# Kernel tuning notes

Hardware: AMD Instinct MI355X
Metric: run time of the kernel (lower is better)

Reference implementation:

```python
import jax, jax.numpy as jnp
import numpy as np

G, K1, K2, N, NP, EPS = 16, 128, 32, 128, 512, 1e-5

def _bn(x, axes):
    m = jnp.mean(x, axes, keepdims=True)
    v = jnp.var(x, axes, keepdims=True)  # biased, as torch BN training mode
    return (x - m) * jax.lax.rsqrt(v + EPS)

def _fps(xyz, npoint):
    # farthest point sampling, deterministic start at index 0; xyz (B,P,3)
    B, P, _ = xyz.shape
    def step(carry, _):
        dists, far = carry
        c = jnp.take_along_axis(xyz, far[:, None, None], axis=1)   # (B,1,3)
        d = jnp.sum((xyz - c) ** 2, -1)                            # (B,P)
        dists = jnp.minimum(dists, d)
        return (dists, jnp.argmax(dists, -1)), far
    init = (jnp.full((B, P), 1e10, xyz.dtype), jnp.zeros((B,), jnp.int32))
    _, idx = jax.lax.scan(step, init, None, length=npoint)         # (npoint,B)
    return jnp.take_along_axis(xyz, idx.T[:, :, None], axis=1)     # (B,npoint,3)

def _pointnet(x, w1, b1, w2, b2, w3, b3):
    h = jax.nn.relu(_bn(x @ w1 + b1, (0, 1)))
    h = jax.nn.relu(_bn(h @ w2 + b2, (0, 1)))
    h = _bn(h @ w3 + b3, (0, 1))
    return jnp.max(h, axis=1)                                      # (B,1024)

def _mapping(feat, w1, b1, w2, b2, w3, b3, w4, b4):
    # all 16 branches stacked on leading axis g
    h = jax.nn.relu(_bn(jnp.einsum('bk,gkj->gbj', feat, w1) + b1[:, None, :], (1,)))
    h = jax.nn.relu(_bn(jnp.einsum('gbj,gjk->gbk', h, w2) + b2[:, None, :], (1,)))
    h = jax.nn.relu(_bn(jnp.einsum('gbj,gjk->gbk', h, w3) + b3[:, None, :], (1,)))
    return jax.nn.relu(_bn(jnp.einsum('gbj,gjk->gbk', h, w4) + b4[:, None, :], (1,)))

def _axform(feat, fw, fb, c1w, c1b, c2w, c2b, c3w, c3b, c4w, c4b):
    # feat (G,B,K1); 1x1 convs expressed as einsums in channels-last layout
    xb = (jnp.einsum('gbk,gkm->gbm', feat, fw) + fb[:, None, :]).reshape(G, -1, N, K2)
    h = jax.nn.relu(_bn(jnp.einsum('gbnk,gkc->gbnc', xb, c1w) + c1b[:, None, None, :], (1, 2)))
    h = jax.nn.relu(_bn(jnp.einsum('gbnc,gcd->gbnd', h, c2w) + c2b[:, None, None, :], (1, 2)))
    h = jnp.einsum('gbnd,gde->gbne', h, c3w) + c3b[:, None, None, :]  # (G,B,N,1024)
    w = jax.nn.softmax(h, axis=2)                                     # softmax over N
    y = jnp.einsum('gbne,gbnk->gbek', w, xb)                          # (G,B,1024,K2)
    return jnp.einsum('gbek,gkc->gbec', y, c4w) + c4b[:, None, None, :]  # (G,B,1024,3)

def _forward(x, pn, mp, gen, ref):
    x_partial = _fps(x, NP)                                           # (B,512,3)
    feat = _pointnet(x, *pn)                                          # (B,1024)
    mfeat = _mapping(feat, *mp)                                       # (G,B,K1)
    x1g = _axform(mfeat, *gen)                                        # (G,B,1024,3)
    B = x.shape[0]
    x_1 = jnp.transpose(x1g, (1, 0, 2, 3)).reshape(B, -1, 3)          # (B,16384,3)
    fps1 = jax.vmap(lambda p: _fps(p, NP))(x1g)                       # (G,B,512,3)
    x_base = jnp.concatenate([fps1, jnp.broadcast_to(x_partial, (G,) + x_partial.shape)], axis=2)
    x2g = x_base + _axform(mfeat, *ref)                               # (G,B,1024,3)
    x_2 = jnp.transpose(x2g, (1, 0, 2, 3)).reshape(B, -1, 3)
    return x_1, x_2

def setup_inputs() -> dict:
    keys = iter(jax.random.split(jax.random.key(0), 40))
    def rn(shape, s=0.02):
        return (s * jax.random.normal(next(keys), shape)).astype(jnp.float32)
    inp = {}
    inp['x'] = jax.random.normal(next(keys), (16, 2048, 3), jnp.float32)
    inp['pn_w1'] = rn((3, 64));      inp['pn_b1'] = rn((64,))
    inp['pn_w2'] = rn((64, 128));    inp['pn_b2'] = rn((128,))
    inp['pn_w3'] = rn((128, 1024));  inp['pn_b3'] = rn((1024,))
    inp['mp_w1'] = rn((G, 1024, 1024)); inp['mp_b1'] = rn((G, 1024))
    inp['mp_w2'] = rn((G, 1024, 1024)); inp['mp_b2'] = rn((G, 1024))
    inp['mp_w3'] = rn((G, 1024, 1024)); inp['mp_b3'] = rn((G, 1024))
    inp['mp_w4'] = rn((G, 1024, K1));   inp['mp_b4'] = rn((G, K1))
    for p in ('g', 'r'):
        inp[p + '_fw'] = rn((G, K1, N * K2)); inp[p + '_fb'] = rn((G, N * K2))
        inp[p + '_c1w'] = rn((G, K2, 64));    inp[p + '_c1b'] = rn((G, 64))
        inp[p + '_c2w'] = rn((G, 64, 128));   inp[p + '_c2b'] = rn((G, 128))
        inp[p + '_c3w'] = rn((G, 128, 1024)); inp[p + '_c3b'] = rn((G, 1024))
        inp[p + '_c4w'] = rn((G, K2, 3));     inp[p + '_c4b'] = rn((G, 3))
    return inp

def reference(x, pn_w1, pn_b1, pn_w2, pn_b2, pn_w3, pn_b3,
              mp_w1, mp_b1, mp_w2, mp_b2, mp_w3, mp_b3, mp_w4, mp_b4,
              g_fw, g_fb, g_c1w, g_c1b, g_c2w, g_c2b, g_c3w, g_c3b, g_c4w, g_c4b,
              r_fw, r_fb, r_c1w, r_c1b, r_c2w, r_c2b, r_c3w, r_c3b, r_c4w, r_c4b):
    pn = (pn_w1, pn_b1, pn_w2, pn_b2, pn_w3, pn_b3)
    mp = (mp_w1, mp_b1, mp_w2, mp_b2, mp_w3, mp_b3, mp_w4, mp_b4)
    gen = (g_fw, g_fb, g_c1w, g_c1b, g_c2w, g_c2b, g_c3w, g_c3b, g_c4w, g_c4b)
    ref = (r_fw, r_fb, r_c1w, r_c1b, r_c2w, r_c2b, r_c3w, r_c3b, r_c4w, r_c4b)
    return _forward(x, pn, mp, gen, ref)
```

## Files before the change

kernel.cpp:

```cpp
#include <hip/hip_runtime.h>
#include <math.h>

#define TID ((int)threadIdx.x)

namespace {
constexpr float EPSf = 1e-5f;

typedef __attribute__((ext_vector_type(8))) short short8;
typedef __attribute__((ext_vector_type(4))) float f32x4;

struct FpsArgs {
  const float* pts; float* out; float* dmin; int* far;
  int it0, it1, nc;
};

__device__ __forceinline__ unsigned fenc(float f){
  unsigned u = __float_as_uint(f);
  return (u & 0x80000000u) ? ~u : (u | 0x80000000u);
}
__device__ __forceinline__ float fdec(unsigned e){
  unsigned u = (e & 0x80000000u) ? (e & 0x7fffffffu) : ~e;
  return __uint_as_float(u);
}
__device__ __forceinline__ short bf16rne(float f){
  unsigned u = __float_as_uint(f);
  return (short)((u + 0x7fffu + ((u >> 16) & 1u)) >> 16);
}

template<int CTRL>
__device__ __forceinline__ void dpp_comb(float& bm, int& bp){
  int om_i = __builtin_amdgcn_update_dpp(__float_as_int(bm), __float_as_int(bm), CTRL, 0xf, 0xf, false);
  int op   = __builtin_amdgcn_update_dpp(bp, bp, CTRL, 0xf, 0xf, false);
  float om = __int_as_float(om_i);
  if (om > bm || (om == bm && op < bp)){ bm = om; bp = op; }
}

template<int LP, int NT>
__device__ void fps_body(const FpsArgs& a, int ci){
  const int NPTS = NT*LP;
  const float* pts = a.pts + (size_t)ci * NPTS * 3;
  float* out = a.out + (size_t)ci * 512 * 3;
  float* dst = a.dmin + (size_t)ci * NPTS;
  float px[LP], py[LP], pz[LP], dmin[LP];
#pragma unroll
  for (int j = 0; j < LP; j++){
    int p = TID + NT*j;
    px[j] = pts[p*3+0]; py[j] = pts[p*3+1]; pz[j] = pts[p*3+2];
  }
  int far;
  if (a.it0 == 0){
#pragma unroll
    for (int j = 0; j < LP; j++) dmin[j] = 1e10f;
    far = 0;
  } else {
#pragma unroll
    for (int j = 0; j < LP; j++) dmin[j] = dst[TID + NT*j];
    far = a.far[ci];
  }
  __shared__ unsigned long long red2[2][NT/64];
  for (int i = a.it0; i < a.it1; i++){
    float cx = pts[far*3+0], cy = pts[far*3+1], cz = pts[far*3+2];
    if (TID == 0){ out[i*3+0]=cx; out[i*3+1]=cy; out[i*3+2]=cz; }
    float bm = -1.f; int bp = 0;
#pragma unroll
    for (int j = 0; j < LP; j++){
      float dx = __fsub_rn(px[j], cx);
      float dy = __fsub_rn(py[j], cy);
      float dz = __fsub_rn(pz[j], cz);
      float d  = __fadd_rn(__fadd_rn(__fmul_rn(dx,dx), __fmul_rn(dy,dy)), __fmul_rn(dz,dz));
      float dm = fminf(dmin[j], d);
      dmin[j] = dm;
      if (dm > bm){ bm = dm; bp = TID + NT*j; }
    }
    dpp_comb<0x111>(bm,bp); dpp_comb<0x112>(bm,bp); dpp_comb<0x114>(bm,bp);
    dpp_comb<0x118>(bm,bp); dpp_comb<0x142>(bm,bp); dpp_comb<0x143>(bm,bp);
    unsigned long long key =
      ((unsigned long long)(unsigned)__builtin_amdgcn_readlane(__float_as_int(bm), 63) << 32)
      | (unsigned)~(unsigned)__builtin_amdgcn_readlane(bp, 63);
    if ((TID & 63) == 63) red2[i&1][TID>>6] = key;
    __syncthreads();
    unsigned long long kk = red2[i&1][0];
#pragma unroll
    for (int t = 1; t < NT/64; t++){
      unsigned long long o = red2[i&1][t];
      kk = kk > o ? kk : o;
    }
    far = (int)~(unsigned)kk;
  }
  if (a.it1 < 512){
#pragma unroll
    for (int j = 0; j < LP; j++) dst[TID + NT*j] = dmin[j];
    if (TID == 0) a.far[ci] = far;
  }
}

template<int C, int K, int FLP>
__global__ void __launch_bounds__(256) rowgemm_kernel(const float* __restrict__ in,
    const float* __restrict__ w, const float* __restrict__ bias, const float2* __restrict__ st2,
    float* __restrict__ out, int rows_per_g, FpsArgs fa)
{
  int bid = blockIdx.x;
  if constexpr (FLP > 0){
    if (bid < fa.nc){ fps_body<FLP,256>(fa, bid); return; }
    bid -= fa.nc;
  }
  constexpr int RPB = 256 / C;
  __shared__ float lin[RPB * K];
  size_t row0 = (size_t)bid * RPB;
  int g = (int)(row0 / rows_per_g);
  for (int i = TID; i < RPB*K; i += 256){
    float v = in[row0*(size_t)K + i];
    if (st2){ float2 s = st2[(size_t)g*K + (i % K)]; v = fmaxf((v - s.x)*s.y, 0.f); }
    lin[i] = v;
  }
  __syncthreads();
  int r = TID / C, c = TID % C;
  float acc = bias[(size_t)g*C + c];
  const float* wg = w + (size_t)g*K*C + c;
#pragma unroll
  for (int k = 0; k < K; k++) acc = fmaf(lin[r*K + k], wg[(size_t)k*C], acc);
  out[(row0 + r)*C + c] = acc;
}

template<int FLP>
__global__ void __launch_bounds__(256, 4) big1024b_kernel(const float* __restrict__ in,
    const float* __restrict__ w, const float* __restrict__ bias, const float2* __restrict__ st2,
    float* __restrict__ ps, float* __restrict__ pq, unsigned* __restrict__ maxenc, FpsArgs fa)
{
  int bid = blockIdx.x;
  if constexpr (FLP > 0){
    if (bid < fa.nc){ fps_body<FLP,256>(fa, bid); return; }
    bid -= fa.nc;
  }
  int rb = bid >> 1, ch = bid & 1;
  size_t row0 = (size_t)rb * 32;
  __shared__ float linT[4096];
  for (int i = TID; i < 4096; i += 256){
    int r = i >> 7, k = i & 127;
    float v = in[(row0 + r)*128 + k];
    float2 s = st2[k];
    linT[k*32 + r] = fmaxf((v - s.x)*s.y, 0.f);
  }
  __syncthreads();
  int rq = TID >> 6, cq = TID & 63;
  int c0 = ch*512 + cq*8;
  float acc[8][8];
  {
    float4 b0 = *(const float4*)(bias + c0);
    float4 b1 = *(const float4*)(bias + c0 + 4);
    const float bv[8] = {b0.x,b0.y,b0.z,b0.w,b1.x,b1.y,b1.z,b1.w};
#pragma unroll
    for (int ri = 0; ri < 8; ri++)
#pragma unroll
      for (int ci = 0; ci < 8; ci++) acc[ri][ci] = bv[ci];
  }
  const float* wp = w + c0;
#pragma unroll 2
  for (int k = 0; k < 128; k++){
    float4 w0 = *(const float4*)(wp + (size_t)k*1024);
    float4 w1 = *(const float4*)(wp + (size_t)k*1024 + 4);
    float4 l0 = *(const float4*)&linT[k*32 + rq*8];
    float4 l1 = *(const float4*)&linT[k*32 + rq*8 + 4];
    const float lv[8] = {l0.x,l0.y,l0.z,l0.w,l1.x,l1.y,l1.z,l1.w};
    const float wv[8] = {w0.x,w0.y,w0.z,w0.w,w1.x,w1.y,w1.z,w1.w};
#pragma unroll
    for (int ri = 0; ri < 8; ri++)
#pragma unroll
      for (int ci = 0; ci < 8; ci++)
        acc[ri][ci] = fmaf(lv[ri], wv[ci], acc[ri][ci]);
  }
  float s[8], q[8], m[8];
#pragma unroll
  for (int ci = 0; ci < 8; ci++){
    s[ci] = 0.f; q[ci] = 0.f; m[ci] = -1e38f;
#pragma unroll
    for (int ri = 0; ri < 8; ri++){
      float v = acc[ri][ci];
      s[ci] += v; q[ci] = fmaf(v, v, q[ci]); m[ci] = fmaxf(m[ci], v);
    }
  }
  __syncthreads();
  float* red = linT;
#pragma unroll
  for (int ci = 0; ci < 8; ci++){
    red[rq*512 + cq*8 + ci]        = s[ci];
    red[2048 + rq*512 + cq*8 + ci] = q[ci];
  }
  __syncthreads();
  if (rq == 0){
#pragma unroll
    for (int ci = 0; ci < 8; ci++){
      float ss = 0.f, qq = 0.f;
#pragma unroll
      for (int r = 0; r < 4; r++){
        ss += red[r*512 + cq*8 + ci];
        qq += red[2048 + r*512 + cq*8 + ci];
      }
      ps[(size_t)rb*1024 + c0 + ci] = ss;
      pq[(size_t)rb*1024 + c0 + ci] = qq;
    }
  }
  __syncthreads();
#pragma unroll
  for (int ci = 0; ci < 8; ci++) red[rq*512 + cq*8 + ci] = m[ci];
  __syncthreads();
  if (rq == 0){
    int b = (int)(row0 / 2048);
#pragma unroll
    for (int ci = 0; ci < 8; ci++){
      float mm = red[cq*8 + ci];
#pragma unroll
      for (int r = 1; r < 4; r++) mm = fmaxf(mm, red[r*512 + cq*8 + ci]);
      atomicMax(&maxenc[(size_t)b*1024 + c0 + ci], fenc(mm));
    }
  }
}

template<int FLP>
__global__ void __launch_bounds__(128) mapgemm2_kernel(const float* __restrict__ in, int in_gstride,
    const float* __restrict__ w, const float* __restrict__ bias, const float2* __restrict__ st2,
    float* __restrict__ out, int K, int J, int JB, int NS, FpsArgs fa)
{
  int bid = blockIdx.x;
  if constexpr (FLP > 0){
    if (bid < fa.nc){ fps_body<FLP,128>(fa, bid); return; }
    bid -= fa.nc;
  }
  int kc = bid / (JB*16);
  int g  = (bid / JB) % 16;
  int jb = bid % JB;
  int kchunk = K / NS, k0 = kc*kchunk;
  __shared__ float linT[128*16];
  const float* ing = in + (size_t)g * in_gstride;
  for (int i = TID; i < kchunk*16; i += 128){
    int b = i / kchunk, k = i - b*kchunk;
    float v = ing[(size_t)b*K + k0 + k];
    if (st2){ float2 s = st2[(size_t)g*K + k0 + k]; v = fmaxf((v - s.x)*s.y, 0.f); }
    linT[k*16 + b] = v;
  }
  __syncthreads();
  int bh = TID >> 6, jq = TID & 63;
  int j = jb*256 + jq*4;
  const float* wp = w + ((size_t)g*K + k0)*J + j;
  float4 a4[8];
#pragma unroll
  for (int bi = 0; bi < 8; bi++) a4[bi] = make_float4(0.f,0.f,0.f,0.f);
#pragma unroll 4
  for (int k = 0; k < kchunk; k++){
    float4 wv = *(const float4*)(wp + (size_t)k*J);
    float4 l0 = *(const float4*)&linT[k*16 + bh*8];
    float4 l1 = *(const float4*)&linT[k*16 + bh*8 + 4];
    const float lv[8] = {l0.x,l0.y,l0.z,l0.w,l1.x,l1.y,l1.z,l1.w};
#pragma unroll
    for (int bi = 0; bi < 8; bi++){
      a4[bi].x = fmaf(lv[bi], wv.x, a4[bi].x);
      a4[bi].y = fmaf(lv[bi], wv.y, a4[bi].y);
      a4[bi].z = fmaf(lv[bi], wv.z, a4[bi].z);
      a4[bi].w = fmaf(lv[bi], wv.w, a4[bi].w);
    }
  }
  if (NS == 1){
    float4 bv = *(const float4*)(bias + (size_t)g*J + j);
#pragma unroll
    for (int bi = 0; bi < 8; bi++){
      int b = bh*8 + bi;
      float4 o = make_float4(a4[bi].x+bv.x, a4[bi].y+bv.y, a4[bi].z+bv.z, a4[bi].w+bv.w);
      *(float4*)&out[((size_t)g*16 + b)*J + j] = o;
    }
  } else {
#pragma unroll
    for (int bi = 0; bi < 8; bi++)
      *(float4*)&out[(((size_t)kc*16 + g)*16 + bh*8 + bi)*J + j] = a4[bi];
  }
}

__global__ void __launch_bounds__(256) mapgemm_kernel(const float* __restrict__ in, int in_gstride,
    const float* __restrict__ w, const float* __restrict__ bias, const float2* __restrict__ st2,
    float* __restrict__ out, int K, int J, int JB, int NS)
{
  int bid = blockIdx.x;
  int kc = bid / (JB*16);
  int g  = (bid / JB) % 16;
  int jb = bid % JB;
  int j  = jb*256 + TID;
  bool jv = j < J;
  int jc = jv ? j : 0;
  int kchunk = K / NS;
  int k0 = kc * kchunk;
  __shared__ float lin[16 * 128];
  const float* ing = in + (size_t)g * in_gstride;
  float acc[16];
  float bv = (NS == 1 && jv) ? bias[(size_t)g*J + jc] : 0.f;
#pragma unroll
  for (int b = 0; b < 16; b++) acc[b] = bv;
  for (int kt = k0; kt < k0 + kchunk; kt += 128){
    __syncthreads();
    for (int i = TID; i < 2048; i += 256){
      int b = i >> 7, k = i & 127;
      float v = ing[(size_t)b*K + kt + k];
      if (st2){ float2 s = st2[(size_t)g*K + kt + k]; v = fmaxf((v - s.x)*s.y, 0.f); }
      lin[i] = v;
    }
    __syncthreads();
    const float* wg = w + ((size_t)g*K + kt)*J + jc;
    for (int k = 0; k < 128; k++){
      float wv = wg[(size_t)k*J];
#pragma unroll
      for (int b = 0; b < 16; b++) acc[b] = fmaf(lin[b*128 + k], wv, acc[b]);
    }
  }
  if (jv){
    if (NS == 1){
      for (int b = 0; b < 16; b++) out[((size_t)g*16 + b)*J + j] = acc[b];
    } else {
      for (int b = 0; b < 16; b++) out[(((size_t)kc*16 + g)*16 + b)*J + j] = acc[b];
    }
  }
}

__global__ void __launch_bounds__(256) redstats_kernel(const float* __restrict__ part,
    const float* __restrict__ bias, float* __restrict__ out, float2* __restrict__ st2,
    int J, int NS)
{
  int t = blockIdx.x*256 + TID;
  int g = t / J, j = t % J;
  float bv = bias[t];
  float s = 0.f, q = 0.f;
  for (int b = 0; b < 16; b++){
    float v = bv;
    for (int c = 0; c < NS; c++) v += part[(((size_t)c*16 + g)*16 + b)*J + j];
    out[((size_t)g*16 + b)*J + j] = v;
    s += v; q = fmaf(v, v, q);
  }
  float mean = s * (1.f/16.f);
  float var  = q * (1.f/16.f) - mean*mean;
  st2[t] = make_float2(mean, rsqrtf(fmaxf(var, 0.f) + EPSf));
}

template<int FLP>
__global__ void __launch_bounds__(256) statsacc_kernel(const float* __restrict__ in,
    float* __restrict__ part, int C, size_t chunk, FpsArgs fa)
{
  int bid = blockIdx.x;
  if constexpr (FLP > 0){
    if (bid < fa.nc){ fps_body<FLP,256>(fa, bid); return; }
    bid -= fa.nc;
  }
  size_t base = (size_t)bid * chunk;
  int c = TID % C;
  float s = 0.f, q = 0.f;
  for (size_t idx = base + TID; idx < base + chunk; idx += 256){
    float v = in[idx]; s += v; q = fmaf(v, v, q);
  }
  __shared__ float ls[256], lq[256];
  ls[TID] = s; lq[TID] = q; __syncthreads();
  if (TID < C){
    for (int t = TID + C; t < 256; t += C){ s += ls[t]; q += lq[t]; }
    part[((size_t)bid*C + c)*2]   = s;
    part[((size_t)bid*C + c)*2+1] = q;
  }
}

__global__ void statsfin_kernel(const float* __restrict__ part, float2* __restrict__ st2,
    int C, int G, float invR)
{
  int slot = blockIdx.x*256 + TID;
  if (slot >= G*C) return;
  int g = slot / C, c = slot % C;
  int bpg = 256 / G;
  float s = 0.f, q = 0.f;
  for (int b = 0; b < bpg; b++){
    size_t p = ((size_t)(g*bpg + b)*C + c)*2;
    s += part[p]; q += part[p+1];
  }
  float mean = s*invR;
  float var  = q*invR - mean*mean;
  st2[slot] = make_float2(mean, rsqrtf(fmaxf(var, 0.f) + EPSf));
}

__global__ void pnfin_kernel(const float* __restrict__ ps, const float* __restrict__ pq,
                             float2* __restrict__ st)
{
  int c = blockIdx.x*256 + TID;
  float s = 0.f, q = 0.f;
  for (int rb = 0; rb < 1024; rb++){ s += ps[rb*1024 + c]; q += pq[rb*1024 + c]; }
  float mean = s * (1.f/32768.f);
  float var  = q * (1.f/32768.f) - mean*mean;
  st[c] = make_float2(mean, rsqrtf(fmaxf(var, 0.f) + EPSf));
}

__global__ void feat_kernel(const unsigned* __restrict__ me, const float2* __restrict__ st,
                            float* __restrict__ feat)
{
  int t = blockIdx.x*256 + TID;
  int c = t & 1023;
  float2 s = st[c];
  feat[t] = (fdec(me[t]) - s.x) * s.y;
}

__global__ void __launch_bounds__(256) wtr_kernel(const float* __restrict__ c3w,
                                                  short* __restrict__ wt)
{
  int g = blockIdx.x >> 4, kt = blockIdx.x & 15;
  __shared__ float lds[8*1024];
  const float* src = c3w + ((size_t)g*128 + kt*8)*1024;
  for (int i = TID; i < 8192; i += 256) lds[i] = src[i];
  __syncthreads();
  for (int e = TID; e < 1024; e += 256){
    short8 v;
#pragma unroll
    for (int j = 0; j < 8; j++) v[j] = bf16rne(lds[j*1024 + e]);
    *(short8*)&wt[((size_t)g*1024 + e)*128 + kt*8] = v;
  }
}

template<int FLP>
__global__ void __launch_bounds__(256, 3) fused_kernel(const float* __restrict__ c2o,
    const float2* __restrict__ st2, const short* __restrict__ wt,
    const float* __restrict__ xb, const float* __restrict__ c4w, const float* __restrict__ c4b,
    float* __restrict__ out_pts, float* __restrict__ out_x1, FpsArgs fa)
{
  int bid = blockIdx.x;
  if constexpr (FLP > 0){
    if (bid < fa.nc){ fps_body<FLP,256>(fa, bid); return; }
    bid -= fa.nc;
  }
  int gb = bid >> 3, eb = bid & 7;
  int g = gb >> 4, b = gb & 15;
  __shared__ short Abf[16384];
  __shared__ short xbT[4096];
  __shared__ float mred[512];
  __shared__ float sred[128];

  {
    const float* xsrc = xb + (size_t)gb*4096;
    for (int idx = TID; idx < 1024; idx += 256){
      int n = idx >> 3, k4 = (idx & 7)*4;
      float4 v = *(const float4*)(xsrc + n*32 + k4);
      const float vv[4] = {v.x, v.y, v.z, v.w};
#pragma unroll
      for (int j = 0; j < 4; j++){
        int k = k4 + j;
        xbT[k*128 + (((n >> 3) ^ (k & 7)) << 3) + (n & 7)] = bf16rne(vv[j]);
      }
    }
  }
  const float* src = c2o + (size_t)gb*16384;
  for (int i = TID; i < 2048; i += 256){
    int n = i >> 4, kc = i & 15;
    float4 a0 = *(const float4*)(src + n*128 + kc*8);
    float4 a1 = *(const float4*)(src + n*128 + kc*8 + 4);
    const float vals[8] = {a0.x,a0.y,a0.z,a0.w,a1.x,a1.y,a1.z,a1.w};
    short8 ob;
#pragma unroll
    for (int j = 0; j < 8; j++){
      float2 s = st2[(size_t)g*128 + kc*8 + j];
      ob[j] = bf16rne(fmaxf((vals[j] - s.x)*s.y, 0.f));
    }
    *(short8*)&Abf[n*128 + ((kc ^ (n & 7)) << 3)] = ob;
  }
  __syncthreads();

  int lane = TID & 63, wid = TID >> 6;
  int lr = lane & 15, lkg = lane >> 4;

  f32x4 acc[2][8];
#pragma unroll
  for (int nt = 0; nt < 2; nt++)
#pragma unroll
    for (int et = 0; et < 8; et++) acc[nt][et] = (f32x4){0.f,0.f,0.f,0.f};
  const short* wtg = wt + ((size_t)g*1024 + eb*128)*128;
#pragma unroll
  for (int kt = 0; kt < 4; kt++){
    int kb = kt*32 + lkg*8;
    int kcf = kb >> 3;
    short8 afr[2];
#pragma unroll
    for (int nt = 0; nt < 2; nt++){
      int row = wid*32 + nt*16 + lr;
      afr[nt] = *(const short8*)&Abf[row*128 + ((kcf ^ (row & 7)) << 3)];
    }
#pragma unroll
    for (int et = 0; et < 8; et++){
      short8 bfr = *(const short8*)&wtg[(et*16 + lr)*128 + kb];
      acc[0][et] = __builtin_amdgcn_mfma_f32_16x16x32_bf16(afr[0], bfr, acc[0][et], 0, 0, 0);
      acc[1][et] = __builtin_amdgcn_mfma_f32_16x16x32_bf16(afr[1], bfr, acc[1][et], 0, 0, 0);
    }
  }

  float m[8];
#pragma unroll
  for (int et = 0; et < 8; et++){
    float mm = -1e38f;
#pragma unroll
    for (int nt = 0; nt < 2; nt++)
#pragma unroll
      for (int r = 0; r < 4; r++) mm = fmaxf(mm, acc[nt][et][r]);
    mm = fmaxf(mm, __shfl_xor(mm, 16));
    mm = fmaxf(mm, __shfl_xor(mm, 32));
    m[et] = mm;
  }
  if (lkg == 0){
#pragma unroll
    for (int et = 0; et < 8; et++) mred[wid*128 + et*16 + lr] = m[et];
  }
  __syncthreads();
#pragma unroll
  for (int et = 0; et < 8; et++){
    float mm = fmaxf(fmaxf(mred[et*16 + lr],       mred[128 + et*16 + lr]),
                     fmaxf(mred[256 + et*16 + lr], mred[384 + et*16 + lr]));
    m[et] = mm;
  }

  float sp[8];
  unsigned* Pu = (unsigned*)Abf;
#pragma unroll
  for (int et = 0; et < 8; et++){
    float ss = 0.f;
#pragma unroll
    for (int nt = 0; nt < 2; nt++)
#pragma unroll
      for (int r = 0; r < 4; r++){
        float p = __expf(acc[nt][et][r] - m[et]);
        acc[nt][et][r] = p;
        ss += p;
      }
    ss += __shfl_xor(ss, 16);
    ss += __shfl_xor(ss, 32);
    sp[et] = ss;
    int e = et*16 + lr;
#pragma unroll
    for (int nt = 0; nt < 2; nt++){
      int nb = wid*32 + nt*16 + lkg*4;
      int base = e*128 + ((((nb >> 3)) ^ (e & 7)) << 3) + (nb & 7);
      unsigned lo = (unsigned)(unsigned short)bf16rne(acc[nt][et][0])
                  | ((unsigned)(unsigned short)bf16rne(acc[nt][et][1]) << 16);
      unsigned hi = (unsigned)(unsigned short)bf16rne(acc[nt][et][2])
                  | ((unsigned)(unsigned short)bf16rne(acc[nt][et][3]) << 16);
      Pu[base >> 1]       = lo;
      Pu[(base >> 1) + 1] = hi;
    }
  }
  __syncthreads();
  if (lkg == 0){
#pragma unroll
    for (int et = 0; et < 8; et++) mred[wid*128 + et*16 + lr] = sp[et];
  }
  __syncthreads();
  if (wid == 0){
#pragma unroll
    for (int t = 0; t < 2; t++){
      int e = t*64 + lane;
      float s = mred[e] + mred[128 + e] + mred[256 + e] + mred[384 + e];
      sred[e] = 1.f / s;
    }
  }

  f32x4 yy[2][2];
#pragma unroll
  for (int t2 = 0; t2 < 2; t2++){ yy[t2][0] = (f32x4){0.f,0.f,0.f,0.f}; yy[t2][1] = (f32x4){0.f,0.f,0.f,0.f}; }
#pragma unroll
  for (int nc = 0; nc < 4; nc++){
    short8 bfrs[2];
#pragma unroll
    for (int kt2 = 0; kt2 < 2; kt2++){
      int k = kt2*16 + lr;
      bfrs[kt2] = *(const short8*)&xbT[k*128 + (((nc*4 + lkg) ^ (k & 7)) << 3)];
    }
#pragma unroll
    for (int t2 = 0; t2 < 2; t2++){
      int e = (wid*2 + t2)*16 + lr;
      short8 afr = *(const short8*)&Abf[e*128 + (((nc*4 + lkg) ^ (e & 7)) << 3)];
      yy[t2][0] = __builtin_amdgcn_mfma_f32_16x16x32_bf16(afr, bfrs[0], yy[t2][0], 0, 0, 0);
      yy[t2][1] = __builtin_amdgcn_mfma_f32_16x16x32_bf16(afr, bfrs[1], yy[t2][1], 0, 0, 0);
    }
  }
  __syncthreads();

  float c4l[2][3];
  {
    const float* cw = c4w + g*96;
#pragma unroll
    for (int kt2 = 0; kt2 < 2; kt2++){
      int k = kt2*16 + lr;
      c4l[kt2][0] = cw[k*3+0]; c4l[kt2][1] = cw[k*3+1]; c4l[kt2][2] = cw[k*3+2];
    }
  }
  float cb0 = c4b[g*3+0], cb1 = c4b[g*3+1], cb2 = c4b[g*3+2];
#pragma unroll
  for (int t2 = 0; t2 < 2; t2++){
#pragma unroll
    for (int r = 0; r < 4; r++){
      float o0 = yy[t2][0][r]*c4l[0][0] + yy[t2][1][r]*c4l[1][0];
      float o1 = yy[t2][0][r]*c4l[0][1] + yy[t2][1][r]*c4l[1][1];
      float o2 = yy[t2][0][r]*c4l[0][2] + yy[t2][1][r]*c4l[1][2];
#pragma unroll
      for (int d = 1; d < 16; d <<= 1){
        o0 += __shfl_xor(o0, d);
        o1 += __shfl_xor(o1, d);
        o2 += __shfl_xor(o2, d);
      }
      if (lr == 0){
        int e = (wid*2 + t2)*16 + lkg*4 + r;
        float rs = sred[e];
        o0 = fmaf(o0, rs, cb0);
        o1 = fmaf(o1, rs, cb1);
        o2 = fmaf(o2, rs, cb2);
        int eg = eb*128 + e;
        size_t po = ((size_t)gb*1024 + eg)*3;
        out_pts[po+0] = o0; out_pts[po+1] = o1; out_pts[po+2] = o2;
        if (out_x1){
          size_t xo = (((size_t)b*16 + g)*1024 + eg)*3;
          out_x1[xo+0] = o0; out_x1[xo+1] = o1; out_x1[xo+2] = o2;
        }
      }
    }
  }
}

__global__ void combine_kernel(const float* __restrict__ fps1, const float* __restrict__ xpart,
                               const float* __restrict__ d2, float* __restrict__ x2)
{
  size_t i = (size_t)blockIdx.x*256 + TID;
  if (i >= (size_t)16*16*1024*3) return;
  int c = (int)(i % 3);
  size_t t = i / 3;
  int e = (int)(t % 1024);
  size_t gb = t / 1024;
  int g = (int)(gb >> 4), b = (int)(gb & 15);
  float base;
  if (e < 512) base = fps1[(gb*512 + e)*3 + c];
  else         base = xpart[((size_t)b*512 + (e - 512))*3 + c];
  x2[(((size_t)b*16384) + (size_t)g*1024 + e)*3 + c] = base + d2[i];
}

}

extern "C" void kernel_launch(void* const* d_in, const int* in_sizes, int n_in,
                              void* d_out, int out_size, void* d_ws, size_t ws_size,
                              hipStream_t stream)
{
  (void)in_sizes; (void)n_in; (void)out_size; (void)ws_size;
  const float* x    = (const float*)d_in[0];
  const float* pnw1 = (const float*)d_in[1];
  const float* pnb1 = (const float*)d_in[2];
  const float* pnw2 = (const float*)d_in[3];
  const float* pnb2 = (const float*)d_in[4];
  const float* pnw3 = (const float*)d_in[5];
  const float* pnb3 = (const float*)d_in[6];
  const float* mpw[4] = {(const float*)d_in[7],(const float*)d_in[9],(const float*)d_in[11],(const float*)d_in[13]};
  const float* mpb[4] = {(const float*)d_in[8],(const float*)d_in[10],(const float*)d_in[12],(const float*)d_in[14]};

  float* ws = (float*)d_ws;
  size_t o = 0;
  auto alloc = [&](size_t n){ float* p = ws + o; o += n; return p; };
  float* x_partial = alloc(24576);
  float* feat      = alloc(16384);
  float* mfeat     = alloc(32768);
  float2* st_pn1   = (float2*)alloc(128);
  float2* st_pn2   = (float2*)alloc(256);
  float2* st_pn3   = (float2*)alloc(2048);
  float2* st_c1    = (float2*)alloc(2048);
  float2* st_c2    = (float2*)alloc(4096);
  float2* st_map0  = (float2*)alloc(32768);
  float2* st_map1  = (float2*)alloc(32768);
  float2* st_map2  = (float2*)alloc(32768);
  float2* st_map3  = (float2*)alloc(4096);
  float* sa_part   = alloc(65536);
  float* pn_ps     = alloc(1048576);
  float* pn_pq     = alloc(1048576);
  unsigned* maxenc = (unsigned*)alloc(16384);
  float* mapA      = alloc(262144);
  float* mapB      = alloc(262144);
  float* mpart     = alloc(4194304);
  float* xb        = alloc(1048576);
  float* c1o       = alloc(2097152);
  float* c2o       = alloc(4194304);
  float* x1g       = alloc(786432);
  float* d2buf     = alloc(786432);
  float* fps1b     = alloc(393216);
  float* fpsA_dmin = alloc(32768);
  int*   fpsA_far  = (int*)alloc(16);
  float* fpsB_dmin = alloc(262144);
  int*   fpsB_far  = (int*)alloc(256);
  short* wt_g      = (short*)alloc(1048576);
  short* wt_r      = (short*)alloc(1048576);

  float* xout1 = (float*)d_out;
  float* xout2 = xout1 + 786432;

  hipMemsetAsync(maxenc, 0, 16384*sizeof(unsigned), stream);

  wtr_kernel<<<256, 256, 0, stream>>>((const float*)d_in[21], wt_g);
  wtr_kernel<<<256, 256, 0, stream>>>((const float*)d_in[31], wt_r);

  FpsArgs f0{};
  FpsArgs fa{x, x_partial, fpsA_dmin, fpsA_far, 0, 0, 16};

  fa.it0 = 0; fa.it1 = 64;
  rowgemm_kernel<64,3,8><<<8192+16, 256, 0, stream>>>(x, pnw1, pnb1, nullptr, c1o, 32768, fa);
  statsacc_kernel<0><<<256, 256, 0, stream>>>(c1o, sa_part, 64, 8192, f0);
  statsfin_kernel<<<1, 256, 0, stream>>>(sa_part, st_pn1, 64, 1, 1.f/32768.f);
  fa.it0 = 64; fa.it1 = 128;
  rowgemm_kernel<128,64,8><<<16384+16, 256, 0, stream>>>(c1o, pnw2, pnb2, st_pn1, c2o, 32768, fa);
  statsacc_kernel<0><<<256, 256, 0, stream>>>(c2o, sa_part, 128, 16384, f0);
  statsfin_kernel<<<1, 256, 0, stream>>>(sa_part, st_pn2, 128, 1, 1.f/32768.f);
  fa.it0 = 128; fa.it1 = 224;
  big1024b_kernel<8><<<2048+16, 256, 0, stream>>>(c2o, pnw3, pnb3, st_pn2,
                                                  pn_ps, pn_pq, maxenc, fa);
  pnfin_kernel<<<4, 256, 0, stream>>>(pn_ps, pn_pq, st_pn3);
  feat_kernel<<<64, 256, 0, stream>>>(maxenc, st_pn3, feat);

  fa.it0 = 224; fa.it1 = 288;
  mapgemm2_kernel<16><<<1024+16, 128, 0, stream>>>(feat, 0,     mpw[0], nullptr, nullptr, mpart, 1024, 1024, 4, 16, fa);
  redstats_kernel<<<64, 256, 0, stream>>>(mpart, mpb[0], mapA, st_map0, 1024, 16);
  fa.it0 = 288; fa.it1 = 352;
  mapgemm2_kernel<16><<<1024+16, 128, 0, stream>>>(mapA, 16384, mpw[1], nullptr, st_map0, mpart, 1024, 1024, 4, 16, fa);
  redstats_kernel<<<64, 256, 0, stream>>>(mpart, mpb[1], mapB, st_map1, 1024, 16);
  fa.it0 = 352; fa.it1 = 416;
  mapgemm2_kernel<16><<<1024+16, 128, 0, stream>>>(mapB, 16384, mpw[2], nullptr, st_map1, mpart, 1024, 1024, 4, 16, fa);
  redstats_kernel<<<64, 256, 0, stream>>>(mpart, mpb[2], mapA, st_map2, 1024, 16);
  mapgemm_kernel<<<64, 256, 0, stream>>>(mapA, 16384, mpw[3], nullptr, st_map2, mpart, 1024, 128, 1, 4);
  redstats_kernel<<<8, 256, 0, stream>>>(mpart, mpb[3], mfeat, st_map3, 128, 4);

  for (int p = 0; p < 2; p++){
    const float* fw  = (const float*)d_in[15 + p*10 + 0];
    const float* fb  = (const float*)d_in[15 + p*10 + 1];
    const float* c1w = (const float*)d_in[15 + p*10 + 2];
    const float* c1b = (const float*)d_in[15 + p*10 + 3];
    const float* c2w = (const float*)d_in[15 + p*10 + 4];
    const float* c2b = (const float*)d_in[15 + p*10 + 5];
    const float* c4w = (const float*)d_in[15 + p*10 + 8];
    const float* c4b = (const float*)d_in[15 + p*10 + 9];

    if (p == 0){
      fa.it0 = 416; fa.it1 = 480;
      mapgemm2_kernel<16><<<256+16, 128, 0, stream>>>(mfeat, 2048, fw, fb, st_map3, xb, 128, 4096, 16, 1, fa);
      fa.it0 = 480; fa.it1 = 512;
      rowgemm_kernel<64,32,8><<<8192+16, 256, 0, stream>>>(xb, c1w, c1b, nullptr, c1o, 2048, fa);
      statsacc_kernel<0><<<256, 256, 0, stream>>>(c1o, sa_part, 64, 8192, f0);
      statsfin_kernel<<<4, 256, 0, stream>>>(sa_part, st_c1, 64, 16, 1.f/2048.f);
      rowgemm_kernel<128,64,0><<<16384, 256, 0, stream>>>(c1o, c2w, c2b, st_c1, c2o, 2048, f0);
      statsacc_kernel<0><<<256, 256, 0, stream>>>(c2o, sa_part, 128, 16384, f0);
      statsfin_kernel<<<8, 256, 0, stream>>>(sa_part, st_c2, 128, 16, 1.f/2048.f);
      fused_kernel<0><<<2048, 256, 0, stream>>>(c2o, st_c2, wt_g, xb, c4w, c4b, x1g, xout1, f0);
    } else {
      FpsArgs fb_{x1g, fps1b, fpsB_dmin, fpsB_far, 0, 0, 256};
      mapgemm2_kernel<0><<<256, 128, 0, stream>>>(mfeat, 2048, fw, fb, st_map3, xb, 128, 4096, 16, 1, f0);
      fb_.it0 = 0; fb_.it1 = 72;
      rowgemm_kernel<64,32,4><<<8192+256, 256, 0, stream>>>(xb, c1w, c1b, nullptr, c1o, 2048, fb_);
      fb_.it0 = 72; fb_.it1 = 104;
      statsacc_kernel<4><<<256+256, 256, 0, stream>>>(c1o, sa_part, 64, 8192, fb_);
      statsfin_kernel<<<4, 256, 0, stream>>>(sa_part, st_c1, 64, 16, 1.f/2048.f);
      fb_.it0 = 104; fb_.it1 = 208;
      rowgemm_kernel<128,64,4><<<16384+256, 256, 0, stream>>>(c1o, c2w, c2b, st_c1, c2o, 2048, fb_);
      fb_.it0 = 208; fb_.it1 = 240;
      statsacc_kernel<4><<<256+256, 256, 0, stream>>>(c2o, sa_part, 128, 16384, fb_);
      statsfin_kernel<<<8, 256, 0, stream>>>(sa_part, st_c2, 128, 16, 1.f/2048.f);
      fb_.it0 = 240; fb_.it1 = 512;
      fused_kernel<4><<<2048+256, 256, 0, stream>>>(c2o, st_c2, wt_r, xb, c4w, c4b, d2buf, nullptr, fb_);
    }
  }

  combine_kernel<<<3072, 256, 0, stream>>>(fps1b, x_partial, d2buf, xout2);
}
```

Baseline: 1.794 ms.

## Loop fused kernel over all e-blocks per gb and rebalance FPS overlap

```diff
diff --git a/kernel.cpp b/kernel.cpp
--- a/kernel.cpp
+++ b/kernel.cpp
@@ -425,13 +425,15 @@
     if (bid < fa.nc){ fps_body<FLP,256>(fa, bid); return; }
     bid -= fa.nc;
   }
-  int gb = bid >> 3, eb = bid & 7;
+  int gb = bid;
   int g = gb >> 4, b = gb & 15;
-  __shared__ short Abf[16384];
+  __shared__ short Pbf[16384];
   __shared__ short xbT[4096];
+  __shared__ float2 sb[128];
   __shared__ float mred[512];
   __shared__ float sred[128];
 
+  if (TID < 128) sb[TID] = st2[(size_t)g*128 + TID];
   {
     const float* xsrc = xb + (size_t)gb*4096;
     for (int idx = TID; idx < 1024; idx += 256){
@@ -445,137 +447,32 @@
       }
     }
   }
-  const float* src = c2o + (size_t)gb*16384;
-  for (int i = TID; i < 2048; i += 256){
-    int n = i >> 4, kc = i & 15;
-    float4 a0 = *(const float4*)(src + n*128 + kc*8);
-    float4 a1 = *(const float4*)(src + n*128 + kc*8 + 4);
-    const float vals[8] = {a0.x,a0.y,a0.z,a0.w,a1.x,a1.y,a1.z,a1.w};
-    short8 ob;
-#pragma unroll
-    for (int j = 0; j < 8; j++){
-      float2 s = st2[(size_t)g*128 + kc*8 + j];
-      ob[j] = bf16rne(fmaxf((vals[j] - s.x)*s.y, 0.f));
-    }
-    *(short8*)&Abf[n*128 + ((kc ^ (n & 7)) << 3)] = ob;
-  }
   __syncthreads();
 
   int lane = TID & 63, wid = TID >> 6;
   int lr = lane & 15, lkg = lane >> 4;
 
-  f32x4 acc[2][8];
-#pragma unroll
-  for (int nt = 0; nt < 2; nt++)
-#pragma unroll
-    for (int et = 0; et < 8; et++) acc[nt][et] = (f32x4){0.f,0.f,0.f,0.f};
-  const short* wtg = wt + ((size_t)g*1024 + eb*128)*128;
+  short8 afr[4][2];
+  const float* src = c2o + (size_t)gb*16384;
 #pragma unroll
   for (int kt = 0; kt < 4; kt++){
     int kb = kt*32 + lkg*8;
-    int kcf = kb >> 3;
-    short8 afr[2];
+    float2 ss[8];
+#pragma unroll
+    for (int j = 0; j < 8; j++) ss[j] = sb[kb + j];
 #pragma unroll
     for (int nt = 0; nt < 2; nt++){
       int row = wid*32 + nt*16 + lr;
-      afr[nt] = *(const short8*)&Abf[row*128 + ((kcf ^ (row & 7)) << 3)];
-    }
-#pragma unroll
-    for (int et = 0; et < 8; et++){
-      short8 bfr = *(const short8*)&wtg[(et*16 + lr)*128 + kb];
-      acc[0][et] = __builtin_amdgcn_mfma_f32_16x16x32_bf16(afr[0], bfr, acc[0][et], 0, 0, 0);
-      acc[1][et] = __builtin_amdgcn_mfma_f32_16x16x32_bf16(afr[1], bfr, acc[1][et], 0, 0, 0);
-    }
-  }
-
-  float m[8];
-#pragma unroll
-  for (int et = 0; et < 8; et++){
-    float mm = -1e38f;
-#pragma unroll
-    for (int nt = 0; nt < 2; nt++)
-#pragma unroll
-      for (int r = 0; r < 4; r++) mm = fmaxf(mm, acc[nt][et][r]);
-    mm = fmaxf(mm, __shfl_xor(mm, 16));
-    mm = fmaxf(mm, __shfl_xor(mm, 32));
-    m[et] = mm;
-  }
-  if (lkg == 0){
-#pragma unroll
-    for (int et = 0; et < 8; et++) mred[wid*128 + et*16 + lr] = m[et];
-  }
-  __syncthreads();
-#pragma unroll
-  for (int et = 0; et < 8; et++){
-    float mm = fmaxf(fmaxf(mred[et*16 + lr],       mred[128 + et*16 + lr]),
-                     fmaxf(mred[256 + et*16 + lr], mred[384 + et*16 + lr]));
-    m[et] = mm;
-  }
-
-  float sp[8];
-  unsigned* Pu = (unsigned*)Abf;
-#pragma unroll
-  for (int et = 0; et < 8; et++){
-    float ss = 0.f;
-#pragma unroll
-    for (int nt = 0; nt < 2; nt++)
-#pragma unroll
-      for (int r = 0; r < 4; r++){
-        float p = __expf(acc[nt][et][r] - m[et]);
-        acc[nt][et][r] = p;
-        ss += p;
-      }
-    ss += __shfl_xor(ss, 16);
-    ss += __shfl_xor(ss, 32);
-    sp[et] = ss;
-    int e = et*16 + lr;
-#pragma unroll
-    for (int nt = 0; nt < 2; nt++){
-      int nb = wid*32 + nt*16 + lkg*4;
-      int base = e*128 + ((((nb >> 3)) ^ (e & 7)) << 3) + (nb & 7);
-      unsigned lo = (unsigned)(unsigned short)bf16rne(acc[nt][et][0])
-                  | ((unsigned)(unsigned short)bf16rne(acc[nt][et][1]) << 16);
-      unsigned hi = (unsigned)(unsigned short)bf16rne(acc[nt][et][2])
-                  | ((unsigned)(unsigned short)bf16rne(acc[nt][et][3]) << 16);
-      Pu[base >> 1]       = lo;
-      Pu[(base >> 1) + 1] = hi;
-    }
-  }
-  __syncthreads();
-  if (lkg == 0){
-#pragma unroll
-    for (int et = 0; et < 8; et++) mred[wid*128 + et*16 + lr] = sp[et];
-  }
-  __syncthreads();
-  if (wid == 0){
-#pragma unroll
-    for (int t = 0; t < 2; t++){
-      int e = t*64 + lane;
-      float s = mred[e] + mred[128 + e] + mred[256 + e] + mred[384 + e];
-      sred[e] = 1.f / s;
-    }
-  }
-
-  f32x4 yy[2][2];
-#pragma unroll
-  for (int t2 = 0; t2 < 2; t2++){ yy[t2][0] = (f32x4){0.f,0.f,0.f,0.f}; yy[t2][1] = (f32x4){0.f,0.f,0.f,0.f}; }
-#pragma unroll
-  for (int nc = 0; nc < 4; nc++){
-    short8 bfrs[2];
-#pragma unroll
-    for (int kt2 = 0; kt2 < 2; kt2++){
-      int k = kt2*16 + lr;
-      bfrs[kt2] = *(const short8*)&xbT[k*128 + (((nc*4 + lkg) ^ (k & 7)) << 3)];
-    }
-#pragma unroll
-    for (int t2 = 0; t2 < 2; t2++){
-      int e = (wid*2 + t2)*16 + lr;
-      short8 afr = *(const short8*)&Abf[e*128 + (((nc*4 + lkg) ^ (e & 7)) << 3)];
-      yy[t2][0] = __builtin_amdgcn_mfma_f32_16x16x32_bf16(afr, bfrs[0], yy[t2][0], 0, 0, 0);
-      yy[t2][1] = __builtin_amdgcn_mfma_f32_16x16x32_bf16(afr, bfrs[1], yy[t2][1], 0, 0, 0);
-    }
-  }
-  __syncthreads();
+      float4 a0 = *(const float4*)(src + row*128 + kb);
+      float4 a1 = *(const float4*)(src + row*128 + kb + 4);
+      const float vals[8] = {a0.x,a0.y,a0.z,a0.w,a1.x,a1.y,a1.z,a1.w};
+      short8 ob;
+#pragma unroll
+      for (int j = 0; j < 8; j++)
+        ob[j] = bf16rne(fmaxf((vals[j] - ss[j].x)*ss[j].y, 0.f));
+      afr[kt][nt] = ob;
+    }
+  }
 
   float c4l[2][3];
   {
@@ -587,31 +484,139 @@
     }
   }
   float cb0 = c4b[g*3+0], cb1 = c4b[g*3+1], cb2 = c4b[g*3+2];
-#pragma unroll
-  for (int t2 = 0; t2 < 2; t2++){
-#pragma unroll
-    for (int r = 0; r < 4; r++){
-      float o0 = yy[t2][0][r]*c4l[0][0] + yy[t2][1][r]*c4l[1][0];
-      float o1 = yy[t2][0][r]*c4l[0][1] + yy[t2][1][r]*c4l[1][1];
-      float o2 = yy[t2][0][r]*c4l[0][2] + yy[t2][1][r]*c4l[1][2];
-#pragma unroll
-      for (int d = 1; d < 16; d <<= 1){
-        o0 += __shfl_xor(o0, d);
-        o1 += __shfl_xor(o1, d);
-        o2 += __shfl_xor(o2, d);
+  unsigned* Pu = (unsigned*)Pbf;
+
+  for (int eb = 0; eb < 8; eb++){
+    f32x4 acc[2][8];
+#pragma unroll
+    for (int nt = 0; nt < 2; nt++)
+#pragma unroll
+      for (int et = 0; et < 8; et++) acc[nt][et] = (f32x4){0.f,0.f,0.f,0.f};
+    const short* wtg = wt + ((size_t)g*1024 + eb*128)*128;
+#pragma unroll
+    for (int kt = 0; kt < 4; kt++){
+      int kb = kt*32 + lkg*8;
+#pragma unroll
+      for (int et = 0; et < 8; et++){
+        short8 bfr = *(const short8*)&wtg[(et*16 + lr)*128 + kb];
+        acc[0][et] = __builtin_amdgcn_mfma_f32_16x16x32_bf16(afr[kt][0], bfr, acc[0][et], 0, 0, 0);
+        acc[1][et] = __builtin_amdgcn_mfma_f32_16x16x32_bf16(afr[kt][1], bfr, acc[1][et], 0, 0, 0);
       }
-      if (lr == 0){
-        int e = (wid*2 + t2)*16 + lkg*4 + r;
-        float rs = sred[e];
-        o0 = fmaf(o0, rs, cb0);
-        o1 = fmaf(o1, rs, cb1);
-        o2 = fmaf(o2, rs, cb2);
-        int eg = eb*128 + e;
-        size_t po = ((size_t)gb*1024 + eg)*3;
-        out_pts[po+0] = o0; out_pts[po+1] = o1; out_pts[po+2] = o2;
-        if (out_x1){
-          size_t xo = (((size_t)b*16 + g)*1024 + eg)*3;
-          out_x1[xo+0] = o0; out_x1[xo+1] = o1; out_x1[xo+2] = o2;
+    }
+
+    float m[8];
+#pragma unroll
+    for (int et = 0; et < 8; et++){
+      float mm = -1e38f;
+#pragma unroll
+      for (int nt = 0; nt < 2; nt++)
+#pragma unroll
+        for (int r = 0; r < 4; r++) mm = fmaxf(mm, acc[nt][et][r]);
+      mm = fmaxf(mm, __shfl_xor(mm, 16));
+      mm = fmaxf(mm, __shfl_xor(mm, 32));
+      m[et] = mm;
+    }
+    if (lkg == 0){
+#pragma unroll
+      for (int et = 0; et < 8; et++) mred[wid*128 + et*16 + lr] = m[et];
+    }
+    __syncthreads();
+#pragma unroll
+    for (int et = 0; et < 8; et++){
+      m[et] = fmaxf(fmaxf(mred[et*16 + lr],       mred[128 + et*16 + lr]),
+                    fmaxf(mred[256 + et*16 + lr], mred[384 + et*16 + lr]));
+    }
+
+    float sp[8];
+#pragma unroll
+    for (int et = 0; et < 8; et++){
+      float ss = 0.f;
+#pragma unroll
+      for (int nt = 0; nt < 2; nt++)
+#pragma unroll
+        for (int r = 0; r < 4; r++){
+          float p = __expf(acc[nt][et][r] - m[et]);
+          acc[nt][et][r] = p;
+          ss += p;
+        }
+      ss += __shfl_xor(ss, 16);
+      ss += __shfl_xor(ss, 32);
+      sp[et] = ss;
+      int e = et*16 + lr;
+#pragma unroll
+      for (int nt = 0; nt < 2; nt++){
+        int nb = wid*32 + nt*16 + lkg*4;
+        int base = e*128 + ((((nb >> 3)) ^ (e & 7)) << 3) + (nb & 7);
+        unsigned lo = (unsigned)(unsigned short)bf16rne(acc[nt][et][0])
+                    | ((unsigned)(unsigned short)bf16rne(acc[nt][et][1]) << 16);
+        unsigned hi = (unsigned)(unsigned short)bf16rne(acc[nt][et][2])
+                    | ((unsigned)(unsigned short)bf16rne(acc[nt][et][3]) << 16);
+        Pu[base >> 1]       = lo;
+        Pu[(base >> 1) + 1] = hi;
+      }
+    }
+    __syncthreads();
+    if (lkg == 0){
+#pragma unroll
+      for (int et = 0; et < 8; et++) mred[wid*128 + et*16 + lr] = sp[et];
+    }
+    __syncthreads();
+    if (wid == 0){
+#pragma unroll
+      for (int t = 0; t < 2; t++){
+        int e = t*64 + lane;
+        float s = mred[e] + mred[128 + e] + mred[256 + e] + mred[384 + e];
+        sred[e] = 1.f / s;
+      }
+    }
+
+    f32x4 yy[2][2];
+#pragma unroll
+    for (int t2 = 0; t2 < 2; t2++){ yy[t2][0] = (f32x4){0.f,0.f,0.f,0.f}; yy[t2][1] = (f32x4){0.f,0.f,0.f,0.f}; }
+#pragma unroll
+    for (int nc = 0; nc < 4; nc++){
+      short8 bfrs[2];
+#pragma unroll
+      for (int kt2 = 0; kt2 < 2; kt2++){
+        int k = kt2*16 + lr;
+        bfrs[kt2] = *(const short8*)&xbT[k*128 + (((nc*4 + lkg) ^ (k & 7)) << 3)];
+      }
+#pragma unroll
+      for (int t2 = 0; t2 < 2; t2++){
+        int e = (wid*2 + t2)*16 + lr;
+        short8 afrp = *(const short8*)&Pbf[e*128 + (((nc*4 + lkg) ^ (e & 7)) << 3)];
+        yy[t2][0] = __builtin_amdgcn_mfma_f32_16x16x32_bf16(afrp, bfrs[0], yy[t2][0], 0, 0, 0);
+        yy[t2][1] = __builtin_amdgcn_mfma_f32_16x16x32_bf16(afrp, bfrs[1], yy[t2][1], 0, 0, 0);
+      }
+    }
+    __syncthreads();
+
+#pragma unroll
+    for (int t2 = 0; t2 < 2; t2++){
+#pragma unroll
+      for (int r = 0; r < 4; r++){
+        float o0 = yy[t2][0][r]*c4l[0][0] + yy[t2][1][r]*c4l[1][0];
+        float o1 = yy[t2][0][r]*c4l[0][1] + yy[t2][1][r]*c4l[1][1];
+        float o2 = yy[t2][0][r]*c4l[0][2] + yy[t2][1][r]*c4l[1][2];
+#pragma unroll
+        for (int d = 1; d < 16; d <<= 1){
+          o0 += __shfl_xor(o0, d);
+          o1 += __shfl_xor(o1, d);
+          o2 += __shfl_xor(o2, d);
+        }
+        if (lr == 0){
+          int e = (wid*2 + t2)*16 + lkg*4 + r;
+          float rs = sred[e];
+          o0 = fmaf(o0, rs, cb0);
+          o1 = fmaf(o1, rs, cb1);
+          o2 = fmaf(o2, rs, cb2);
+          int eg = eb*128 + e;
+          size_t po = ((size_t)gb*1024 + eg)*3;
+          out_pts[po+0] = o0; out_pts[po+1] = o1; out_pts[po+2] = o2;
+          if (out_x1){
+            size_t xo = (((size_t)b*16 + g)*1024 + eg)*3;
+            out_x1[xo+0] = o0; out_x1[xo+1] = o1; out_x1[xo+2] = o2;
+          }
         }
       }
     }
@@ -743,22 +748,23 @@
       rowgemm_kernel<128,64,0><<<16384, 256, 0, stream>>>(c1o, c2w, c2b, st_c1, c2o, 2048, f0);
       statsacc_kernel<0><<<256, 256, 0, stream>>>(c2o, sa_part, 128, 16384, f0);
       statsfin_kernel<<<8, 256, 0, stream>>>(sa_part, st_c2, 128, 16, 1.f/2048.f);
-      fused_kernel<0><<<2048, 256, 0, stream>>>(c2o, st_c2, wt_g, xb, c4w, c4b, x1g, xout1, f0);
+      fused_kernel<0><<<256, 256, 0, stream>>>(c2o, st_c2, wt_g, xb, c4w, c4b, x1g, xout1, f0);
     } else {
       FpsArgs fb_{x1g, fps1b, fpsB_dmin, fpsB_far, 0, 0, 256};
-      mapgemm2_kernel<0><<<256, 128, 0, stream>>>(mfeat, 2048, fw, fb, st_map3, xb, 128, 4096, 16, 1, f0);
-      fb_.it0 = 0; fb_.it1 = 72;
+      fb_.it0 = 0; fb_.it1 = 40;
+      mapgemm2_kernel<8><<<256+256, 128, 0, stream>>>(mfeat, 2048, fw, fb, st_map3, xb, 128, 4096, 16, 1, fb_);
+      fb_.it0 = 40; fb_.it1 = 120;
       rowgemm_kernel<64,32,4><<<8192+256, 256, 0, stream>>>(xb, c1w, c1b, nullptr, c1o, 2048, fb_);
-      fb_.it0 = 72; fb_.it1 = 104;
+      fb_.it0 = 120; fb_.it1 = 152;
       statsacc_kernel<4><<<256+256, 256, 0, stream>>>(c1o, sa_part, 64, 8192, fb_);
       statsfin_kernel<<<4, 256, 0, stream>>>(sa_part, st_c1, 64, 16, 1.f/2048.f);
-      fb_.it0 = 104; fb_.it1 = 208;
+      fb_.it0 = 152; fb_.it1 = 260;
       rowgemm_kernel<128,64,4><<<16384+256, 256, 0, stream>>>(c1o, c2w, c2b, st_c1, c2o, 2048, fb_);
-      fb_.it0 = 208; fb_.it1 = 240;
+      fb_.it0 = 260; fb_.it1 = 292;
       statsacc_kernel<4><<<256+256, 256, 0, stream>>>(c2o, sa_part, 128, 16384, fb_);
       statsfin_kernel<<<8, 256, 0, stream>>>(sa_part, st_c2, 128, 16, 1.f/2048.f);
-      fb_.it0 = 240; fb_.it1 = 512;
-      fused_kernel<4><<<2048+256, 256, 0, stream>>>(c2o, st_c2, wt_r, xb, c4w, c4b, d2buf, nullptr, fb_);
+      fb_.it0 = 292; fb_.it1 = 512;
+      fused_kernel<4><<<256+256, 256, 0, stream>>>(c2o, st_c2, wt_r, xb, c4w, c4b, d2buf, nullptr, fb_);
     }
   }
 
```

Result: no change. 1.762 ms (-1.8%).
